# Kernel optimization log

Hardware: AMD Instinct MI355X
Metric: run time of the kernel (lower is better)

The kernel has to match this reference:

```python
import jax, jax.numpy as jnp
import numpy as np

HEADS = 8
DIM_HEAD = 64
SCALE = DIM_HEAD ** -0.5
EPS = 1e-5


def layernorm(t, g, b):
    mu = t.mean(-1, keepdims=True)
    var = ((t - mu) ** 2).mean(-1, keepdims=True)
    return (t - mu) * jax.lax.rsqrt(var + EPS) * g + b


def setup_inputs() -> dict:
    key = jax.random.key(0)
    ks = jax.random.split(key, 12)
    b, n, dim, inner = 2, 2048, 512, HEADS * DIM_HEAD
    s = dim ** -0.5
    return {
        "x": jax.random.normal(ks[0], (b, n, dim), jnp.float32),
        "context": jax.random.normal(ks[1], (b, n, dim), jnp.float32),
        "g_x": jnp.ones((dim,), jnp.float32),
        "b_x": jnp.zeros((dim,), jnp.float32),
        "g_c": jnp.ones((dim,), jnp.float32),
        "b_c": jnp.zeros((dim,), jnp.float32),
        "W_qk": jax.random.normal(ks[2], (dim, inner), jnp.float32) * s,
        "W_cqk": jax.random.normal(ks[3], (dim, inner), jnp.float32) * s,
        "W_v": jax.random.normal(ks[4], (dim, inner), jnp.float32) * s,
        "W_cv": jax.random.normal(ks[5], (dim, inner), jnp.float32) * s,
        "W_out": jax.random.normal(ks[6], (inner, dim), jnp.float32) * s,
        "b_out": jnp.zeros((dim,), jnp.float32),
        "W_cout": jax.random.normal(ks[7], (inner, dim), jnp.float32) * s,
        "b_cout": jnp.zeros((dim,), jnp.float32),
    }


def reference(x, context, g_x, b_x, g_c, b_c, W_qk, W_cqk, W_v, W_cv, W_out, b_out, W_cout, b_cout):
    b, i, _ = x.shape
    j = context.shape[1]
    xn = layernorm(x, g_x, b_x)
    cn = layernorm(context, g_c, b_c)

    def split_heads(t):  # [b, n, h*d] -> [b, h, n, d]
        return t.reshape(t.shape[0], t.shape[1], HEADS, DIM_HEAD).transpose(0, 2, 1, 3)

    qk = split_heads(xn @ W_qk)
    cqk = split_heads(cn @ W_cqk)
    v = split_heads(xn @ W_v)
    cv = split_heads(cn @ W_cv)

    sim = jnp.einsum('bhid,bhjd->bhij', qk, cqk) * SCALE  # [b,h,i,j]
    attn = jax.nn.softmax(sim, axis=-1)           # rows: x attends to context
    context_attn = jax.nn.softmax(sim, axis=-2)   # cols: context attends to x

    out = jnp.einsum('bhij,bhjd->bhid', attn, cv)            # [b,h,i,d]
    context_out = jnp.einsum('bhij,bhid->bhjd', context_attn, v)  # [b,h,j,d]

    def merge_heads(t):  # [b,h,n,d] -> [b,n,h*d]
        return t.transpose(0, 2, 1, 3).reshape(t.shape[0], t.shape[2], HEADS * DIM_HEAD)

    out = merge_heads(out) @ W_out + b_out
    context_out = merge_heads(context_out) @ W_cout + b_cout
    return out, context_out
```

## Files before the change

### kernel.cpp

```cpp
#include <hip/hip_runtime.h>


typedef _Float16 half_t;
typedef __attribute__((ext_vector_type(2))) _Float16 half2v;
typedef __attribute__((ext_vector_type(4))) _Float16 half4v;
typedef __attribute__((ext_vector_type(8))) _Float16 half8v;
typedef __attribute__((ext_vector_type(4))) float floatx4;
typedef __attribute__((ext_vector_type(16))) float floatx16;

#define MFMA16(a, b, c) __builtin_amdgcn_mfma_f32_16x16x32_f16((a), (b), (c), 0, 0, 0)
#define MFMA32(a, b, c) __builtin_amdgcn_mfma_f32_32x32x16_f16((a), (b), (c), 0, 0, 0)

#if defined(__has_builtin)
#if __has_builtin(__builtin_amdgcn_exp2f)
#define EXP2F(x) __builtin_amdgcn_exp2f(x)
#else
#define EXP2F(x) exp2f(x)
#endif
#else
#define EXP2F(x) exp2f(x)
#endif

__device__ __forceinline__ half2v pk2(float a, float b) {
#if defined(__has_builtin) && __has_builtin(__builtin_amdgcn_cvt_pkrtz)
    union { __fp16 __attribute__((ext_vector_type(2))) i; half2v o; } u;
    u.i = __builtin_amdgcn_cvt_pkrtz(a, b);
    return u.o;
#else
    half2v r; r[0] = (half_t)a; r[1] = (half_t)b; return r;
#endif
}

__device__ __forceinline__ void gld16(const half_t* g, half_t* l) {
    __builtin_amdgcn_global_load_lds(
        (const __attribute__((address_space(1))) void*)g,
        (__attribute__((address_space(3))) void*)l, 16, 0, 0);
}

__global__ __launch_bounds__(256) void prep_kernel(
    const float* __restrict__ x, const float* __restrict__ ctx,
    const float* __restrict__ gx, const float* __restrict__ bx,
    const float* __restrict__ gc, const float* __restrict__ bc,
    half_t* __restrict__ xn, half_t* __restrict__ cn,
    const float* __restrict__ W0, const float* __restrict__ W1,
    const float* __restrict__ W2, const float* __restrict__ W3,
    const float* __restrict__ W4, const float* __restrict__ W5,
    half_t* __restrict__ Wt)
{
    __shared__ alignas(16) half_t Ts[128][136];
    const int blk = blockIdx.x;
    const int tid = threadIdx.x;
    const int wave = tid >> 6, lane = tid & 63;

    if (blk < 2048) {
        const int row = blk * 4 + wave;
        const float *src, *g, *b;
        half_t* dst;
        if (row < 4096) {
            src = x + (size_t)row * 512; g = gx; b = bx; dst = xn + (size_t)row * 512;
        } else {
            const size_t r = (size_t)(row - 4096);
            src = ctx + r * 512; g = gc; b = bc; dst = cn + r * 512;
        }
        const float4 a0 = *(const float4*)(src + lane * 4);
        const float4 a1 = *(const float4*)(src + 256 + lane * 4);
        float s = a0.x + a0.y + a0.z + a0.w + a1.x + a1.y + a1.z + a1.w;
        float q = a0.x * a0.x + a0.y * a0.y + a0.z * a0.z + a0.w * a0.w +
                  a1.x * a1.x + a1.y * a1.y + a1.z * a1.z + a1.w * a1.w;
#pragma unroll
        for (int m = 1; m < 64; m <<= 1) {
            s += __shfl_xor(s, m);
            q += __shfl_xor(q, m);
        }
        const float mean = s * (1.0f / 512.0f);
        const float var = q * (1.0f / 512.0f) - mean * mean;
        const float rs = rsqrtf(var + 1e-5f);
        const float4 g0 = *(const float4*)(g + lane * 4);
        const float4 g1 = *(const float4*)(g + 256 + lane * 4);
        const float4 b0 = *(const float4*)(b + lane * 4);
        const float4 b1 = *(const float4*)(b + 256 + lane * 4);
        half4v h0, h1;
        h0[0] = (half_t)((a0.x - mean) * rs * g0.x + b0.x);
        h0[1] = (half_t)((a0.y - mean) * rs * g0.y + b0.y);
        h0[2] = (half_t)((a0.z - mean) * rs * g0.z + b0.z);
        h0[3] = (half_t)((a0.w - mean) * rs * g0.w + b0.w);
        h1[0] = (half_t)((a1.x - mean) * rs * g1.x + b1.x);
        h1[1] = (half_t)((a1.y - mean) * rs * g1.y + b1.y);
        h1[2] = (half_t)((a1.z - mean) * rs * g1.z + b1.z);
        h1[3] = (half_t)((a1.w - mean) * rs * g1.w + b1.w);
        *(half4v*)(dst + lane * 4) = h0;
        *(half4v*)(dst + 256 + lane * 4) = h1;
        return;
    }

    const int b2 = blk - 2048;
    const int mat = b2 >> 4, tile = b2 & 15;
    const float* src;
    switch (mat) {
        case 0: src = W0; break;
        case 1: src = W1; break;
        case 2: src = W2; break;
        case 3: src = W3; break;
        case 4: src = W4; break;
        default: src = W5; break;
    }
    const int tr0 = (tile >> 2) * 128;
    const int tc0 = (tile & 3) * 128;
#pragma unroll
    for (int p = 0; p < 16; ++p) {
        const int idx = p * 256 + tid;
        const int r = idx >> 5, c4 = (idx & 31) * 4;
        const float4 w = *(const float4*)(src + (size_t)(tr0 + r) * 512 + tc0 + c4);
        Ts[c4 + 0][r] = (half_t)w.x;
        Ts[c4 + 1][r] = (half_t)w.y;
        Ts[c4 + 2][r] = (half_t)w.z;
        Ts[c4 + 3][r] = (half_t)w.w;
    }
    __syncthreads();
    half_t* dst = Wt + (size_t)mat * 262144;
#pragma unroll
    for (int p = 0; p < 8; ++p) {
        const int idx = p * 256 + tid;
        const int row = idx >> 4, ch = (idx & 15) * 8;
        *(half8v*)(dst + (size_t)(tc0 + row) * 512 + tr0 + ch) = *(const half8v*)&Ts[row][ch];
    }
}

__global__ __launch_bounds__(256) void gemm_in_kernel(
    const half_t* __restrict__ xn, const half_t* __restrict__ cn,
    const half_t* __restrict__ Wt,
    half_t* __restrict__ qk, half_t* __restrict__ v_t,
    half_t* __restrict__ cqk, half_t* __restrict__ cv_t)
{
    const half_t* A; const half_t* B; half_t* O;
    switch (blockIdx.z) {
        case 0:  A = xn; B = Wt;          O = qk;   break;
        case 1:  A = xn; B = Wt + 262144; O = v_t;  break;
        case 2:  A = cn; B = Wt + 524288; O = cqk;  break;
        default: A = cn; B = Wt + 786432; O = cv_t; break;
    }
    const int tr = blockIdx.z & 1;
    const int mt0 = blockIdx.x * 128;
    const int nt0 = blockIdx.y * 128;

    __shared__ alignas(16) half_t As[128 * 64];
    __shared__ alignas(16) half_t Ws[128 * 64];

    const int tid = threadIdx.x;
    const int wave = tid >> 6, lane = tid & 63;
    const int wr = wave >> 1, wc = wave & 1;
    const int q4 = lane >> 4, c = lane & 15;

    int srow[4], scol[4];
#pragma unroll
    for (int p = 0; p < 4; ++p) {
        const int ofs = p * 4096 + wave * 1024 + lane * 16;
        const int row = ofs >> 7;
        const int pc = (ofs >> 4) & 7;
        srow[p] = row;
        scol[p] = (pc ^ (row & 7)) * 8;
    }

    const half_t* P1 = tr ? As : Ws;
    const half_t* P2 = tr ? Ws : As;

    const floatx4 z4 = {0.f, 0.f, 0.f, 0.f};
    floatx4 acc[4][4];
#pragma unroll
    for (int mt = 0; mt < 4; ++mt)
#pragma unroll
        for (int nt = 0; nt < 4; ++nt) acc[mt][nt] = z4;

    for (int kb = 0; kb < 8; ++kb) {
        const int k0 = kb * 64;
#pragma unroll
        for (int p = 0; p < 4; ++p) {
            const int lofs = p * 2048 + wave * 512;
            gld16(A + (size_t)(mt0 + srow[p]) * 512 + k0 + scol[p], As + lofs);
            gld16(B + (size_t)(nt0 + srow[p]) * 512 + k0 + scol[p], Ws + lofs);
        }
        __syncthreads();
#pragma unroll
        for (int kt = 0; kt < 2; ++kt) {
            half8v f1[4], f2[4];
#pragma unroll
            for (int i = 0; i < 4; ++i) {
                const int r1 = wr * 64 + i * 16 + c;
                const int r2 = wc * 64 + i * 16 + c;
                f1[i] = *(const half8v*)&P1[(r1 << 6) + (((kt * 4 + q4) ^ (r1 & 7)) << 3)];
                f2[i] = *(const half8v*)&P2[(r2 << 6) + (((kt * 4 + q4) ^ (r2 & 7)) << 3)];
            }
#pragma unroll
            for (int mt = 0; mt < 4; ++mt)
#pragma unroll
                for (int nt = 0; nt < 4; ++nt)
                    acc[mt][nt] = MFMA16(f1[mt], f2[nt], acc[mt][nt]);
        }
        __syncthreads();
    }

    const int bb = mt0 >> 11;
    const int nnb = mt0 & 2047;
    if (tr) {
#pragma unroll
        for (int mt = 0; mt < 4; ++mt) {
            const int row = nnb + wr * 64 + mt * 16 + q4 * 4;
#pragma unroll
            for (int nt = 0; nt < 4; ++nt) {
                const int col = nt0 + wc * 64 + nt * 16 + c;
                const int h = col >> 6, dd = col & 63;
                half4v pk;
                pk[0] = (half_t)acc[mt][nt][0];
                pk[1] = (half_t)acc[mt][nt][1];
                pk[2] = (half_t)acc[mt][nt][2];
                pk[3] = (half_t)acc[mt][nt][3];
                *(half4v*)(O + ((size_t)(bb * 8 + h) * 64 + dd) * 2048 + row) = pk;
            }
        }
    } else {
#pragma unroll
        for (int mt = 0; mt < 4; ++mt) {
            const int colw = nt0 + wr * 64 + mt * 16 + q4 * 4;
            const int h = colw >> 6, dd = colw & 63;
#pragma unroll
            for (int nt = 0; nt < 4; ++nt) {
                const int row = nnb + wc * 64 + nt * 16 + c;
                half4v pk;
                pk[0] = (half_t)acc[mt][nt][0];
                pk[1] = (half_t)acc[mt][nt][1];
                pk[2] = (half_t)acc[mt][nt][2];
                pk[3] = (half_t)acc[mt][nt][3];
                *(half4v*)(O + ((size_t)(bb * 8 + h) * 2048 + row) * 64 + dd) = pk;
            }
        }
    }
}

__device__ __forceinline__ void stage_tile32(const half_t* Kt, const half_t* Vt,
                                             half_t* ksb, half_t* cvb,
                                             int wave, int lane)
{
#pragma unroll
    for (int p = 0; p < 4; ++p) {
        const int base = p * 256 + wave * 64;
        const int cidx = base + lane;
        const int R = cidx >> 3, ch = cidx & 7;
        const int gR = (R & ~12) | ((R & 4) << 1) | ((R & 8) >> 1);
        const int ksw = ((R >> 2) ^ (R & 3)) & 7;
        gld16(Kt + (size_t)gR * 64 + ((ch ^ ksw) * 8), ksb + base * 8);
        const int vr = cidx >> 4, vc = cidx & 15;
        gld16(Vt + (size_t)vr * 2048 + ((vc ^ (vr & 15)) * 8), cvb + base * 8);
    }
}

__global__ __launch_bounds__(256, 1) void flash_kernel(
    const half_t* __restrict__ qk, const half_t* __restrict__ cqk,
    const half_t* __restrict__ v_t, const half_t* __restrict__ cv_t,
    float* __restrict__ Pbuf, float* __restrict__ Lbuf)
{
    const int bh = blockIdx.x, it = blockIdx.y;
    const int dir = blockIdx.z >> 1, js = blockIdx.z & 1;
    const half_t* Q  = dir ? cqk : qk;
    const half_t* K  = dir ? qk  : cqk;
    const half_t* VT = dir ? v_t : cv_t;
    const half_t* Qb = Q + (size_t)bh * (2048 * 64);
    const half_t* Kb = K + (size_t)bh * (2048 * 64);
    const half_t* VTb = VT + (size_t)bh * (64 * 2048);
    float* Pb = Pbuf + (size_t)((js * 2 + dir) * 16 + bh) * (2048 * 64);
    float* Lb = Lbuf + (size_t)((js * 2 + dir) * 16 + bh) * 2048;

    __shared__ alignas(16) half_t Ks[2][128 * 64];
    __shared__ alignas(16) half_t CVs[2][64 * 128];

    const int tid = threadIdx.x;
    const int wave = tid >> 6, lane = tid & 63;
    const int h = lane >> 5, i5 = lane & 31;

    half8v qf[2][4];
#pragma unroll
    for (int itile = 0; itile < 2; ++itile)
#pragma unroll
        for (int ks = 0; ks < 4; ++ks) {
            half8v v = *(const half8v*)(Qb +
                (size_t)(it * 256 + wave * 64 + itile * 32 + i5) * 64 + ks * 16 + h * 8);
            qf[itile][ks] = v * (half_t)0.18033688f;
        }

    floatx16 accO[2][2];
    float accL[2] = {0.f, 0.f};
#pragma unroll
    for (int dt = 0; dt < 2; ++dt)
#pragma unroll
        for (int itile = 0; itile < 2; ++itile)
#pragma unroll
            for (int q = 0; q < 16; ++q) accO[dt][itile][q] = 0.f;

    const int jt0 = js * 8;
    stage_tile32(Kb + (size_t)jt0 * 8192, VTb + jt0 * 128, Ks[0], CVs[0], wave, lane);
    __syncthreads();

    const int swk = ((i5 >> 2) ^ (i5 & 3)) & 7;
    const int swv = i5 & 15;

    for (int n = 0; n < 8; ++n) {
        const int jt = jt0 + n;
        const int cur = n & 1;
        if (n < 7)
            stage_tile32(Kb + (size_t)(jt + 1) * 8192, VTb + (size_t)(jt + 1) * 128,
                         Ks[cur ^ 1], CVs[cur ^ 1], wave, lane);
        const half_t* ksld = Ks[cur];
        const half_t* cvld = CVs[cur];

#pragma unroll
        for (int g = 0; g < 4; ++g) {
            const int ksbase = (g * 32 + i5) * 64;
            half8v ka[4];
#pragma unroll
            for (int ks = 0; ks < 4; ++ks)
                ka[ks] = *(const half8v*)&ksld[ksbase + (((ks * 2 + h) ^ swk) << 3)];
            half8v pf[2][2];
#pragma unroll
            for (int itile = 0; itile < 2; ++itile) {
                floatx16 st;
#pragma unroll
                for (int q = 0; q < 16; ++q) st[q] = 0.f;
                st = MFMA32(ka[0], qf[itile][0], st);
                st = MFMA32(ka[1], qf[itile][1], st);
                st = MFMA32(ka[2], qf[itile][2], st);
                st = MFMA32(ka[3], qf[itile][3], st);
                float lsum = 0.f;
#pragma unroll
                for (int s = 0; s < 2; ++s) {
                    float ex[8];
#pragma unroll
                    for (int e = 0; e < 8; ++e) {
                        ex[e] = EXP2F(fminf(st[8 * s + e], 15.0f));
                        lsum += ex[e];
                    }
                    union { half8v v; half2v h2[4]; } u;
                    u.h2[0] = pk2(ex[0], ex[1]);
                    u.h2[1] = pk2(ex[2], ex[3]);
                    u.h2[2] = pk2(ex[4], ex[5]);
                    u.h2[3] = pk2(ex[6], ex[7]);
                    pf[itile][s] = u.v;
                }
                accL[itile] += lsum;
            }
#pragma unroll
            for (int dt = 0; dt < 2; ++dt) {
                const int cvbase = (dt * 32 + i5) * 128;
#pragma unroll
                for (int s = 0; s < 2; ++s) {
                    const half8v cva = *(const half8v*)&cvld[cvbase +
                        (((g * 4 + s * 2 + h) ^ swv) << 3)];
                    accO[dt][0] = MFMA32(cva, pf[0][s], accO[dt][0]);
                    accO[dt][1] = MFMA32(cva, pf[1][s], accO[dt][1]);
                }
            }
        }
        __syncthreads();
    }

#pragma unroll
    for (int itile = 0; itile < 2; ++itile) {
        float l = accL[itile];
        l += __shfl_xor(l, 32);
        const int i = it * 256 + wave * 64 + itile * 32 + i5;
        if (h == 0) Lb[i] = l;
#pragma unroll
        for (int dt = 0; dt < 2; ++dt)
#pragma unroll
            for (int rq = 0; rq < 4; ++rq) {
                float4 o;
                o.x = accO[dt][itile][4 * rq + 0];
                o.y = accO[dt][itile][4 * rq + 1];
                o.z = accO[dt][itile][4 * rq + 2];
                o.w = accO[dt][itile][4 * rq + 3];
                *(float4*)(Pb + (size_t)i * 64 + dt * 32 + 8 * rq + 4 * h) = o;
            }
    }
}

__global__ __launch_bounds__(256) void combine_kernel(
    const float* __restrict__ Pbuf, const float* __restrict__ Lbuf,
    half_t* __restrict__ out_h, half_t* __restrict__ ctx_out_h)
{
    const int tid = threadIdx.x;
    const int rg = blockIdx.x * 16 + (tid >> 4);
    const int q = tid & 15;
    const int i = rg & 2047;
    const int bh = (rg >> 11) & 15;
    const int dir = rg >> 15;

    const size_t pb0 = (size_t)(dir * 16 + bh) * (2048 * 64) + (size_t)i * 64 + q * 4;
    const size_t pb1 = pb0 + (size_t)2 * 16 * 2048 * 64;
    const float4 a0 = *(const float4*)(Pbuf + pb0);
    const float4 a1 = *(const float4*)(Pbuf + pb1);
    const size_t lb0 = (size_t)(dir * 16 + bh) * 2048 + i;
    const float l = Lbuf[lb0] + Lbuf[lb0 + (size_t)2 * 16 * 2048];
    const float rl = 1.0f / l;

    half_t* Out = dir ? ctx_out_h : out_h;
    half4v pk;
    pk[0] = (half_t)((a0.x + a1.x) * rl);
    pk[1] = (half_t)((a0.y + a1.y) * rl);
    pk[2] = (half_t)((a0.z + a1.z) * rl);
    pk[3] = (half_t)((a0.w + a1.w) * rl);
    *(half4v*)(Out + (size_t)(bh >> 3) * 2048 * 512 + (size_t)i * 512 +
               (bh & 7) * 64 + q * 4) = pk;
}

__global__ __launch_bounds__(256) void gemm_out_kernel(
    const half_t* __restrict__ out_h, const half_t* __restrict__ ctx_out_h,
    const half_t* __restrict__ Wt,
    const float* __restrict__ bout, const float* __restrict__ bcout,
    float* __restrict__ dout)
{
    const half_t* A; const half_t* B; const float* bias; float* O;
    if (blockIdx.z == 0) { A = out_h;     B = Wt + 1048576; bias = bout;  O = dout; }
    else                 { A = ctx_out_h; B = Wt + 1310720; bias = bcout; O = dout + 2097152; }

    const int mt0 = blockIdx.x * 64;
    const int nt0 = blockIdx.y * 128;

    __shared__ alignas(16) half_t As[64 * 64];
    __shared__ alignas(16) half_t Ws[128 * 64];

    const int tid = threadIdx.x;
    const int wave = tid >> 6, lane = tid & 63;
    const int wr = wave >> 1, wc = wave & 1;
    const int q4 = lane >> 4, c = lane & 15;

    int srow[4], scol[4];
#pragma unroll
    for (int p = 0; p < 4; ++p) {
        const int ofs = p * 4096 + wave * 1024 + lane * 16;
        const int row = ofs >> 7;
        const int pc = (ofs >> 4) & 7;
        srow[p] = row;
        scol[p] = (pc ^ (row & 7)) * 8;
    }

    const floatx4 z4 = {0.f, 0.f, 0.f, 0.f};
    floatx4 acc[4][2];
#pragma unroll
    for (int mt = 0; mt < 4; ++mt)
#pragma unroll
        for (int nt = 0; nt < 2; ++nt) acc[mt][nt] = z4;

    for (int kb = 0; kb < 8; ++kb) {
        const int k0 = kb * 64;
#pragma unroll
        for (int p = 0; p < 4; ++p) {
            const int lofs = p * 2048 + wave * 512;
            gld16(B + (size_t)(nt0 + srow[p]) * 512 + k0 + scol[p], Ws + lofs);
            if (p < 2)
                gld16(A + (size_t)(mt0 + srow[p]) * 512 + k0 + scol[p], As + lofs);
        }
        __syncthreads();
#pragma unroll
        for (int kt = 0; kt < 2; ++kt) {
            half8v f1[4], f2[2];
#pragma unroll
            for (int i = 0; i < 4; ++i) {
                const int r1 = wr * 64 + i * 16 + c;
                f1[i] = *(const half8v*)&Ws[(r1 << 6) + (((kt * 4 + q4) ^ (r1 & 7)) << 3)];
            }
#pragma unroll
            for (int i = 0; i < 2; ++i) {
                const int r2 = wc * 32 + i * 16 + c;
                f2[i] = *(const half8v*)&As[(r2 << 6) + (((kt * 4 + q4) ^ (r2 & 7)) << 3)];
            }
#pragma unroll
            for (int mt = 0; mt < 4; ++mt)
#pragma unroll
                for (int nt = 0; nt < 2; ++nt)
                    acc[mt][nt] = MFMA16(f1[mt], f2[nt], acc[mt][nt]);
        }
        __syncthreads();
    }

#pragma unroll
    for (int mt = 0; mt < 4; ++mt) {
        const int col = nt0 + wr * 64 + mt * 16 + q4 * 4;
        const float4 bv = *(const float4*)(bias + col);
#pragma unroll
        for (int nt = 0; nt < 2; ++nt) {
            const int row = mt0 + wc * 32 + nt * 16 + c;
            float4 o;
            o.x = acc[mt][nt][0] + bv.x;
            o.y = acc[mt][nt][1] + bv.y;
            o.z = acc[mt][nt][2] + bv.z;
            o.w = acc[mt][nt][3] + bv.w;
            *(float4*)(O + (size_t)row * 512 + col) = o;
        }
    }
}

extern "C" void kernel_launch(void* const* d_in, const int* in_sizes, int n_in,
                              void* d_out, int out_size, void* d_ws, size_t ws_size,
                              hipStream_t stream)
{
    (void)in_sizes; (void)n_in; (void)out_size; (void)ws_size;
    const float* x      = (const float*)d_in[0];
    const float* ctx    = (const float*)d_in[1];
    const float* g_x    = (const float*)d_in[2];
    const float* b_x    = (const float*)d_in[3];
    const float* g_c    = (const float*)d_in[4];
    const float* b_c    = (const float*)d_in[5];
    const float* W_qk   = (const float*)d_in[6];
    const float* W_cqk  = (const float*)d_in[7];
    const float* W_v    = (const float*)d_in[8];
    const float* W_cv   = (const float*)d_in[9];
    const float* W_out  = (const float*)d_in[10];
    const float* b_out  = (const float*)d_in[11];
    const float* W_cout = (const float*)d_in[12];
    const float* b_cout = (const float*)d_in[13];
    float* out = (float*)d_out;

    half_t* ws = (half_t*)d_ws;
    const size_t SEG = 2097152;
    half_t* xn        = ws;
    half_t* cn        = ws + 1 * SEG;
    half_t* qk        = ws + 2 * SEG;
    half_t* cqk       = ws + 3 * SEG;
    half_t* v_t       = ws + 4 * SEG;
    half_t* cv_t      = ws + 5 * SEG;
    half_t* Wt        = ws + 6 * SEG;
    half_t* out_h     = xn;
    half_t* ctx_out_h = cn;
    float* Pbuf = (float*)(ws + 6 * SEG + 1572864);
    float* Lbuf = Pbuf + (size_t)2 * 2 * 16 * 2048 * 64;

    prep_kernel<<<2144, 256, 0, stream>>>(x, ctx, g_x, b_x, g_c, b_c, xn, cn,
                                          W_qk, W_v, W_cqk, W_cv, W_out, W_cout, Wt);
    gemm_in_kernel<<<dim3(32, 4, 4), 256, 0, stream>>>(xn, cn, Wt, qk, v_t, cqk, cv_t);
    flash_kernel<<<dim3(16, 8, 4), 256, 0, stream>>>(qk, cqk, v_t, cv_t, Pbuf, Lbuf);
    combine_kernel<<<4096, 256, 0, stream>>>(Pbuf, Lbuf, out_h, ctx_out_h);
    gemm_out_kernel<<<dim3(64, 4, 2), 256, 0, stream>>>(out_h, ctx_out_h, Wt, b_out, b_cout, out);
}
```

Measured before the change: 193.7 us.

## Shrink flash tiles to raise occupancy and add MFMA priority hints

Each flash block now handles 128 query rows instead of 256, so each wave owns one 32-row tile, and it streams 64-key tiles instead of 128. LDS use falls to 32KB and launch_bounds asks for 4 blocks per CU. The grid doubles to 1024 blocks to cover the whole GPU with more resident waves. s_setprio hints are wrapped around the MFMA sequences. In exchange, K/V reuse per block drops, so global and LDS traffic rise, and there are twice as many barriers per key range.

```diff
diff --git a/kernel.cpp b/kernel.cpp
--- a/kernel.cpp
+++ b/kernel.cpp
@@ -236,24 +236,23 @@
     }
 }
 
-__device__ __forceinline__ void stage_tile32(const half_t* Kt, const half_t* Vt,
+__device__ __forceinline__ void stage_tile64(const half_t* Kt, const half_t* Vt,
                                              half_t* ksb, half_t* cvb,
                                              int wave, int lane)
 {
 #pragma unroll
-    for (int p = 0; p < 4; ++p) {
+    for (int p = 0; p < 2; ++p) {
         const int base = p * 256 + wave * 64;
         const int cidx = base + lane;
         const int R = cidx >> 3, ch = cidx & 7;
         const int gR = (R & ~12) | ((R & 4) << 1) | ((R & 8) >> 1);
         const int ksw = ((R >> 2) ^ (R & 3)) & 7;
         gld16(Kt + (size_t)gR * 64 + ((ch ^ ksw) * 8), ksb + base * 8);
-        const int vr = cidx >> 4, vc = cidx & 15;
-        gld16(Vt + (size_t)vr * 2048 + ((vc ^ (vr & 15)) * 8), cvb + base * 8);
-    }
-}
-
-__global__ __launch_bounds__(256, 1) void flash_kernel(
+        gld16(Vt + (size_t)R * 2048 + ((ch ^ (R & 7)) * 8), cvb + base * 8);
+    }
+}
+
+__global__ __launch_bounds__(256, 4) void flash_kernel(
     const half_t* __restrict__ qk, const half_t* __restrict__ cqk,
     const half_t* __restrict__ v_t, const half_t* __restrict__ cv_t,
     float* __restrict__ Pbuf, float* __restrict__ Lbuf)
@@ -269,113 +268,108 @@
     float* Pb = Pbuf + (size_t)((js * 2 + dir) * 16 + bh) * (2048 * 64);
     float* Lb = Lbuf + (size_t)((js * 2 + dir) * 16 + bh) * 2048;
 
-    __shared__ alignas(16) half_t Ks[2][128 * 64];
-    __shared__ alignas(16) half_t CVs[2][64 * 128];
+    __shared__ alignas(16) half_t Ks[2][64 * 64];
+    __shared__ alignas(16) half_t CVs[2][64 * 64];
 
     const int tid = threadIdx.x;
     const int wave = tid >> 6, lane = tid & 63;
     const int h = lane >> 5, i5 = lane & 31;
 
-    half8v qf[2][4];
-#pragma unroll
-    for (int itile = 0; itile < 2; ++itile)
-#pragma unroll
-        for (int ks = 0; ks < 4; ++ks) {
-            half8v v = *(const half8v*)(Qb +
-                (size_t)(it * 256 + wave * 64 + itile * 32 + i5) * 64 + ks * 16 + h * 8);
-            qf[itile][ks] = v * (half_t)0.18033688f;
-        }
-
-    floatx16 accO[2][2];
-    float accL[2] = {0.f, 0.f};
+    half8v qf[4];
+#pragma unroll
+    for (int ks = 0; ks < 4; ++ks) {
+        half8v v = *(const half8v*)(Qb +
+            (size_t)(it * 128 + wave * 32 + i5) * 64 + ks * 16 + h * 8);
+        qf[ks] = v * (half_t)0.18033688f;
+    }
+
+    floatx16 accO[2];
+    float accL = 0.f;
 #pragma unroll
     for (int dt = 0; dt < 2; ++dt)
 #pragma unroll
-        for (int itile = 0; itile < 2; ++itile)
-#pragma unroll
-            for (int q = 0; q < 16; ++q) accO[dt][itile][q] = 0.f;
-
-    const int jt0 = js * 8;
-    stage_tile32(Kb + (size_t)jt0 * 8192, VTb + jt0 * 128, Ks[0], CVs[0], wave, lane);
+        for (int q = 0; q < 16; ++q) accO[dt][q] = 0.f;
+
+    const int jt0 = js * 16;
+    stage_tile64(Kb + (size_t)jt0 * 4096, VTb + jt0 * 64, Ks[0], CVs[0], wave, lane);
     __syncthreads();
 
     const int swk = ((i5 >> 2) ^ (i5 & 3)) & 7;
-    const int swv = i5 & 15;
-
-    for (int n = 0; n < 8; ++n) {
+    const int swv = i5 & 7;
+
+    for (int n = 0; n < 16; ++n) {
         const int jt = jt0 + n;
         const int cur = n & 1;
-        if (n < 7)
-            stage_tile32(Kb + (size_t)(jt + 1) * 8192, VTb + (size_t)(jt + 1) * 128,
+        if (n < 15)
+            stage_tile64(Kb + (size_t)(jt + 1) * 4096, VTb + (size_t)(jt + 1) * 64,
                          Ks[cur ^ 1], CVs[cur ^ 1], wave, lane);
         const half_t* ksld = Ks[cur];
         const half_t* cvld = CVs[cur];
 
 #pragma unroll
-        for (int g = 0; g < 4; ++g) {
+        for (int g = 0; g < 2; ++g) {
             const int ksbase = (g * 32 + i5) * 64;
             half8v ka[4];
 #pragma unroll
             for (int ks = 0; ks < 4; ++ks)
                 ka[ks] = *(const half8v*)&ksld[ksbase + (((ks * 2 + h) ^ swk) << 3)];
-            half8v pf[2][2];
-#pragma unroll
-            for (int itile = 0; itile < 2; ++itile) {
-                floatx16 st;
-#pragma unroll
-                for (int q = 0; q < 16; ++q) st[q] = 0.f;
-                st = MFMA32(ka[0], qf[itile][0], st);
-                st = MFMA32(ka[1], qf[itile][1], st);
-                st = MFMA32(ka[2], qf[itile][2], st);
-                st = MFMA32(ka[3], qf[itile][3], st);
-                float lsum = 0.f;
-#pragma unroll
-                for (int s = 0; s < 2; ++s) {
-                    float ex[8];
-#pragma unroll
-                    for (int e = 0; e < 8; ++e) {
-                        ex[e] = EXP2F(fminf(st[8 * s + e], 15.0f));
-                        lsum += ex[e];
-                    }
-                    union { half8v v; half2v h2[4]; } u;
-                    u.h2[0] = pk2(ex[0], ex[1]);
-                    u.h2[1] = pk2(ex[2], ex[3]);
-                    u.h2[2] = pk2(ex[4], ex[5]);
-                    u.h2[3] = pk2(ex[6], ex[7]);
-                    pf[itile][s] = u.v;
+            floatx16 st;
+#pragma unroll
+            for (int q = 0; q < 16; ++q) st[q] = 0.f;
+            __builtin_amdgcn_s_setprio(1);
+            st = MFMA32(ka[0], qf[0], st);
+            st = MFMA32(ka[1], qf[1], st);
+            st = MFMA32(ka[2], qf[2], st);
+            st = MFMA32(ka[3], qf[3], st);
+            __builtin_amdgcn_s_setprio(0);
+            half8v pf[2];
+            float lsum = 0.f;
+#pragma unroll
+            for (int s = 0; s < 2; ++s) {
+                float ex[8];
+#pragma unroll
+                for (int e = 0; e < 8; ++e) {
+                    ex[e] = EXP2F(fminf(st[8 * s + e], 15.0f));
+                    lsum += ex[e];
                 }
-                accL[itile] += lsum;
-            }
+                union { half8v v; half2v h2[4]; } u;
+                u.h2[0] = pk2(ex[0], ex[1]);
+                u.h2[1] = pk2(ex[2], ex[3]);
+                u.h2[2] = pk2(ex[4], ex[5]);
+                u.h2[3] = pk2(ex[6], ex[7]);
+                pf[s] = u.v;
+            }
+            accL += lsum;
+            __builtin_amdgcn_s_setprio(1);
 #pragma unroll
             for (int dt = 0; dt < 2; ++dt) {
-                const int cvbase = (dt * 32 + i5) * 128;
+                const int cvbase = (dt * 32 + i5) * 64;
 #pragma unroll
                 for (int s = 0; s < 2; ++s) {
                     const half8v cva = *(const half8v*)&cvld[cvbase +
                         (((g * 4 + s * 2 + h) ^ swv) << 3)];
-                    accO[dt][0] = MFMA32(cva, pf[0][s], accO[dt][0]);
-                    accO[dt][1] = MFMA32(cva, pf[1][s], accO[dt][1]);
+                    accO[dt] = MFMA32(cva, pf[s], accO[dt]);
                 }
             }
+            __builtin_amdgcn_s_setprio(0);
         }
         __syncthreads();
     }
 
-#pragma unroll
-    for (int itile = 0; itile < 2; ++itile) {
-        float l = accL[itile];
+    {
+        float l = accL;
         l += __shfl_xor(l, 32);
-        const int i = it * 256 + wave * 64 + itile * 32 + i5;
+        const int i = it * 128 + wave * 32 + i5;
         if (h == 0) Lb[i] = l;
 #pragma unroll
         for (int dt = 0; dt < 2; ++dt)
 #pragma unroll
             for (int rq = 0; rq < 4; ++rq) {
                 float4 o;
-                o.x = accO[dt][itile][4 * rq + 0];
-                o.y = accO[dt][itile][4 * rq + 1];
-                o.z = accO[dt][itile][4 * rq + 2];
-                o.w = accO[dt][itile][4 * rq + 3];
+                o.x = accO[dt][4 * rq + 0];
+                o.y = accO[dt][4 * rq + 1];
+                o.z = accO[dt][4 * rq + 2];
+                o.w = accO[dt][4 * rq + 3];
                 *(float4*)(Pb + (size_t)i * 64 + dt * 32 + 8 * rq + 4 * h) = o;
             }
     }
@@ -535,7 +529,7 @@
     prep_kernel<<<2144, 256, 0, stream>>>(x, ctx, g_x, b_x, g_c, b_c, xn, cn,
                                           W_qk, W_v, W_cqk, W_cv, W_out, W_cout, Wt);
     gemm_in_kernel<<<dim3(32, 4, 4), 256, 0, stream>>>(xn, cn, Wt, qk, v_t, cqk, cv_t);
-    flash_kernel<<<dim3(16, 8, 4), 256, 0, stream>>>(qk, cqk, v_t, cv_t, Pbuf, Lbuf);
+    flash_kernel<<<dim3(16, 16, 4), 256, 0, stream>>>(qk, cqk, v_t, cv_t, Pbuf, Lbuf);
     combine_kernel<<<4096, 256, 0, stream>>>(Pbuf, Lbuf, out_h, ctx_out_h);
     gemm_out_kernel<<<dim3(64, 4, 2), 256, 0, stream>>>(out_h, ctx_out_h, Wt, b_out, b_cout, out);
 }
```

After: 184.9 us. -4.6%, faster.
